# Optimization experiments

Measured on AMD Instinct MI355X. Metric: run time of the kernel, lower is better.

## Reference

```python
import jax, jax.numpy as jnp
import numpy as np
from jax import lax

# dimension numbers for a true 4D convolution: layout is (N, C, s1, s2, s3, s4)
_DN = lax.ConvDimensionNumbers(lhs_spec=(0, 1, 2, 3, 4, 5),
                               rhs_spec=(0, 1, 2, 3, 4, 5),
                               out_spec=(0, 1, 2, 3, 4, 5))


def _conv4d(x, w, b):
    # x: [B, Cin, H1, W1, H2, W2], w: [Cout, Cin, 3, 3, 3, 3], 'same' padding
    y = lax.conv_general_dilated(x, w, window_strides=(1, 1, 1, 1),
                                 padding='SAME', dimension_numbers=_DN)
    return y + b.reshape(1, -1, 1, 1, 1, 1)


def _ncnet(x, W1, b1, W2, b2, W3, b3):
    h = jax.nn.relu(_conv4d(x, W1, b1))
    h = jax.nn.relu(_conv4d(h, W2, b2))
    h = jax.nn.relu(_conv4d(h, W3, b3))
    return h


def setup_inputs() -> dict:
    key = jax.random.key(0)
    ks = jax.random.split(key, 7)
    B, G = 4, 32  # batch, grid size (H1=W1=H2=W2=G)
    x = jax.random.normal(ks[0], (B, 1, G, G, G, G), dtype=jnp.float32)
    s1 = 1.0 / np.sqrt(1 * 3 ** 4)
    s2 = 1.0 / np.sqrt(10 * 3 ** 4)
    W1 = jax.random.normal(ks[1], (10, 1, 3, 3, 3, 3), dtype=jnp.float32) * s1
    b1 = jax.random.normal(ks[2], (10,), dtype=jnp.float32) * s1
    W2 = jax.random.normal(ks[3], (10, 10, 3, 3, 3, 3), dtype=jnp.float32) * s2
    b2 = jax.random.normal(ks[4], (10,), dtype=jnp.float32) * s2
    W3 = jax.random.normal(ks[5], (1, 10, 3, 3, 3, 3), dtype=jnp.float32) * s2
    b3 = jax.random.normal(ks[6], (1,), dtype=jnp.float32) * s2
    return {"x": x, "W1": W1, "b1": b1, "W2": W2, "b2": b2,
            "W3": W3, "b3": b3}


def reference(x, W1, b1, W2, b2, W3, b3):
    # symmetric mode: f(x) + swap(f(swap(x))) where swap exchanges (H1,W1)<->(H2,W2)
    out_a = _ncnet(x, W1, b1, W2, b2, W3, b3)
    xt = jnp.transpose(x, (0, 1, 4, 5, 2, 3))
    out_b = jnp.transpose(_ncnet(xt, W1, b1, W2, b2, W3, b3),
                          (0, 1, 4, 5, 2, 3))
    return out_a + out_b
```

## Files before the change

### kernel.cpp

```cpp
#include <hip/hip_runtime.h>

#define GSZ 32
#define NPTS (1<<20)

#define XB_FLOATS ((size_t)34*34*34*16)
#define XTP ((size_t)34*34*34*160)

#define OFF_XB  ((size_t)0)
#define OFF_X2  (XB_FLOATS)
#define BSLOT   (XB_FLOATS + 4*XTP + 16)

#define WSB_FLOATS 20480
#define NHALO 6536

typedef __attribute__((ext_vector_type(8)))  short bf16x8;
typedef __attribute__((ext_vector_type(16))) float f32x16;
typedef __attribute__((ext_vector_type(4)))  unsigned uintx4;

__device__ __forceinline__ unsigned short f2bf(float f) {
    union { float f; unsigned u; } v; v.f = f;
    unsigned r = v.u + 0x7FFFu + ((v.u >> 16) & 1u);
    return (unsigned short)(r >> 16);
}

__global__ void k_bpack_all(const float* __restrict__ W1, const float* __restrict__ W2,
                            const float* __restrict__ W3,
                            unsigned* __restrict__ wsB2, unsigned* __restrict__ wsB3,
                            unsigned* __restrict__ wsB1) {
    int t = threadIdx.x;
    int lane = t & 63, j = t >> 6;
    int n = lane & 31, kh = lane >> 5;
    for (int br = 0; br < 2; ++br)
        for (int g = 0; g < 27; ++g) {
            int d1 = g / 9, d2 = (g / 3) % 3, d3 = g % 3;
            unsigned v = 0;
            for (int e = 0; e < 2; ++e) {
                int k = kh * 8 + 2 * j + e;
                unsigned short h = 0;
                if (k < 10 && n < 30) {
                    int co = n % 10, d4 = n / 10;
                    int tap = br == 0 ? ((d1 * 3 + d2) * 3 + d3) * 3 + d4
                                      : ((d3 * 3 + d4) * 3 + d1) * 3 + d2;
                    h = f2bf(W2[(co * 10 + k) * 81 + tap]);
                }
                v |= (unsigned)h << (16 * e);
            }
            wsB2[((br * 27 + g) * 64 + lane) * 4 + j] = v;
        }
    for (int br = 0; br < 2; ++br)
        for (int g = 0; g < 9; ++g) {
            int d1 = g / 3, d2 = g % 3;
            unsigned v = 0;
            for (int e = 0; e < 2; ++e) {
                int k = kh * 8 + 2 * j + e;
                unsigned short h = 0;
                if (k < 10 && n < 9) {
                    int d3 = n / 3, d4 = n % 3;
                    int tap = br == 0 ? ((d1 * 3 + d2) * 3 + d3) * 3 + d4
                                      : ((d3 * 3 + d4) * 3 + d1) * 3 + d2;
                    h = f2bf(W3[k * 81 + tap]);
                }
                v |= (unsigned)h << (16 * e);
            }
            wsB3[((br * 9 + g) * 64 + lane) * 4 + j] = v;
        }
    for (int br = 0; br < 2; ++br)
        for (int g = 0; g < 3; ++g) {
            unsigned v = 0;
            for (int e = 0; e < 2; ++e) {
                int kap = kh * 8 + 2 * j + e;
                unsigned short h = 0;
                if (kap < 9 && n < 30) {
                    int co = n % 10, d4 = n / 10;
                    int d1 = kap / 3, d2 = kap % 3;
                    int tap = br == 0 ? ((d1 * 3 + d2) * 3 + g) * 3 + d4
                                      : ((g * 3 + d4) * 3 + d1) * 3 + d2;
                    h = f2bf(W1[co * 81 + tap]);
                }
                v |= (unsigned)h << (16 * e);
            }
            wsB1[((br * 3 + g) * 64 + lane) * 4 + j] = v;
        }
}

__global__ __launch_bounds__(256) void k_zero_halo(float* __restrict__ ws) {
    int wid = blockIdx.x * 4 + (threadIdx.x >> 6);
    if (wid >= NHALO) return;
    int lane = threadIdx.x & 63;
    int i, j, k;
    if (wid < 2312) {
        i = (wid < 1156) ? 0 : 33;
        int r = wid % 1156; j = r / 34; k = r % 34;
    } else if (wid < 4488) {
        int r = wid - 2312;
        i = 1 + r / 68;
        int r2 = r % 68;
        j = (r2 < 34) ? 0 : 33;
        k = r2 % 34;
    } else {
        int r = wid - 4488;
        i = 1 + r / 64;
        int r2 = r % 64;
        j = 1 + (r2 >> 1);
        k = (r2 & 1) ? 33 : 0;
    }
    size_t line = (size_t)(i * 34 + j) * 34 + k;
    float* slot = ws + (size_t)blockIdx.y * BSLOT;
    uintx4 z4 = {0u, 0u, 0u, 0u};
    if (lane < 40) {
        char* base = (char*)(slot + OFF_X2) + line * 640 + lane * 16;
#pragma unroll
        for (int tns = 0; tns < 4; ++tns)
            *(uintx4*)(base + (size_t)tns * (XTP * 4)) = z4;
    }
    if (lane < 4) ((uintx4*)((char*)(slot + OFF_XB) + line * 64))[lane] = z4;
}

__global__ __launch_bounds__(256) void k_copy_in(const float* __restrict__ x,
                                                 float* __restrict__ ws, int b0) {
    int b = b0 + blockIdx.z;
    int gid = blockIdx.x * 256 + threadIdx.x;
    int l0 = (gid & 7) * 4;
    int k = (gid >> 3) & 31, j = (gid >> 8) & 31, i = gid >> 13;
    float4 v = *(const float4*)(x + (size_t)b * NPTS + (size_t)gid * 4);
    ushort4 h;
    h.x = f2bf(v.x); h.y = f2bf(v.y); h.z = f2bf(v.z); h.w = f2bf(v.w);
    unsigned short* XB = (unsigned short*)(ws + (size_t)blockIdx.z * BSLOT + OFF_XB);
    *(ushort4*)(XB + ((size_t)(((i + 1) * 34 + (j + 1)) * 34 + (k + 1))) * 32 + l0) = h;
}

__global__ __launch_bounds__(256) void k_conv1m(const unsigned* __restrict__ wsB1,
                                                const float* __restrict__ B1,
                                                float* ws) {
    __shared__ float epi[4][34 * 33];
    int t = threadIdx.x, lane = t & 63, wv = t >> 6;
    int zb = blockIdx.z >> 2, br = (blockIdx.z >> 1) & 1, w = blockIdx.z & 1;
    int bid = blockIdx.x;
    int s = ((bid & 7) << 7) | (bid >> 3);
    int i = s >> 5, j = s & 31;
    int k0g = w * 16 + wv * 4;
    int q = lane & 31, half = lane >> 5;

    float bias[8];
#pragma unroll
    for (int e = 0; e < 8; ++e) {
        int co = half * 8 + e;
        bias[e] = (co < 10) ? B1[co] : 0.f;
    }
    if (lane < 33) { epi[wv][lane] = 0.f; epi[wv][33 * 33 + lane] = 0.f; }

    float* slot = ws + (size_t)zb * BSLOT;
    const unsigned short* XB = (const unsigned short*)(slot + OFF_XB);
    const unsigned short* xb = XB + ((size_t)((i * 34 + j) * 34 + k0g)) * 32 + q;
    const bf16x8* Bg = (const bf16x8*)(wsB1 + br * 3 * 64 * 4);

    bf16x8 A[6];
    if (half == 0) {
#pragma unroll
        for (int kk = 0; kk < 6; ++kk) {
            bf16x8 a;
#pragma unroll
            for (int e = 0; e < 8; ++e) {
                const int d1 = e / 3, d2 = e % 3;
                a[e] = (short)xb[(size_t)(d1 * 34 + d2) * 1088 + kk * 32];
            }
            A[kk] = a;
        }
    } else {
#pragma unroll
        for (int kk = 0; kk < 6; ++kk) {
            bf16x8 a = {};
            a[0] = (short)xb[(size_t)(2 * 34 + 2) * 1088 + kk * 32];
            A[kk] = a;
        }
    }
    bf16x8 Bf[3];
#pragma unroll
    for (int d3 = 0; d3 < 3; ++d3) Bf[d3] = Bg[d3 * 64 + lane];

    f32x16 D[4] = {};
#pragma unroll
    for (int kk = 0; kk < 6; ++kk)
#pragma unroll
        for (int m = 0; m < 4; ++m) {
            int d3 = kk - m;
            if (d3 >= 0 && d3 < 3)
                D[m] = __builtin_amdgcn_mfma_f32_32x32x16_bf16(A[kk], Bf[d3], D[m], 0, 0, 0);
        }

    float* epw = epi[wv];
    char* X2b = (char*)(slot + OFF_X2 + (size_t)br * XTP);
#pragma unroll
    for (int m = 0; m < 4; ++m) {
#pragma unroll
        for (int r = 0; r < 16; ++r) {
            int row = (r & 3) + 8 * (r >> 2) + 4 * half;
            epw[(row + 1) * 33 + q] = D[m][r];
        }
        size_t lb = ((size_t)(((i + 1) * 34 + (j + 1)) * 34 + (k0g + m + 1))) * 640 + q * 20;
        if (half == 0) {
            unsigned u[4];
#pragma unroll
            for (int e = 0; e < 4; ++e) {
                unsigned short h2[2];
#pragma unroll
                for (int xx = 0; xx < 2; ++xx) {
                    int co = 2 * e + xx;
                    float v = bias[2 * e + xx];
#pragma unroll
                    for (int ss = 0; ss < 3; ++ss)
                        v += epw[(q + ss) * 33 + ss * 10 + co];
                    h2[xx] = f2bf(fmaxf(v, 0.f));
                }
                u[e] = (unsigned)h2[0] | ((unsigned)h2[1] << 16);
            }
            uintx4 u4 = {u[0], u[1], u[2], u[3]};
            *(uintx4*)(X2b + lb) = u4;
        } else {
            unsigned short h2[2];
#pragma unroll
            for (int xx = 0; xx < 2; ++xx) {
                int co = 8 + xx;
                float v = bias[xx];
#pragma unroll
                for (int ss = 0; ss < 3; ++ss)
                    v += epw[(q + ss) * 33 + ss * 10 + co];
                h2[xx] = f2bf(fmaxf(v, 0.f));
            }
            *(unsigned*)(X2b + lb + 16) = (unsigned)h2[0] | ((unsigned)h2[1] << 16);
        }
    }
}

__global__ __launch_bounds__(256) void k_conv2m(const unsigned* __restrict__ wsB,
                                                const float* __restrict__ B2,
                                                float* ws) {
    __shared__ float epi[4][34 * 33];

    int t = threadIdx.x;
    int lane = t & 63, wv = t >> 6;
    int zb = blockIdx.z >> 2, br = (blockIdx.z >> 1) & 1, w = blockIdx.z & 1;
    int bid = blockIdx.x;
    int s = ((bid & 7) << 7) | (bid >> 3);
    int i = s >> 5, j = s & 31;
    int k0 = (w * 4 + wv) * 4;
    int q = lane & 31, half = lane >> 5;

    if (lane < 33) { epi[wv][lane] = 0.f; epi[wv][33 * 33 + lane] = 0.f; }

    float bias[8];
#pragma unroll
    for (int e = 0; e < 8; ++e) {
        int co = half * 8 + e;
        bias[e] = (co < 10) ? B2[co] : 0.f;
    }

    float* slot = ws + (size_t)zb * BSLOT;
    const char* X2b = (const char*)(slot + OFF_X2 + (size_t)br * XTP)
                      + q * 20 + half * 16 + (size_t)k0 * 640;
    const bf16x8* Bg = (const bf16x8*)(wsB + br * 27 * 64 * 4);

    bf16x8 A[2][6];
#pragma unroll
    for (int kk = 0; kk < 6; ++kk)
        A[0][kk] = *(const bf16x8*)(X2b + ((size_t)(i * 34 + j) * 34) * 640 + kk * 640);

    f32x16 D[4] = {};

#pragma unroll
    for (int g = 0; g < 9; ++g) {
        if (g < 8) {
            const int gn = g + 1, d1n = gn / 3, d2n = gn % 3;
            const char* pn = X2b + ((size_t)((i + d1n) * 34 + (j + d2n)) * 34) * 640;
#pragma unroll
            for (int kk = 0; kk < 6; ++kk)
                A[gn & 1][kk] = *(const bf16x8*)(pn + kk * 640);
        }
        bf16x8 Bf[3];
#pragma unroll
        for (int d3 = 0; d3 < 3; ++d3)
            Bf[d3] = Bg[(g * 3 + d3) * 64 + lane];
#pragma unroll
        for (int kk = 0; kk < 6; ++kk)
#pragma unroll
            for (int m = 0; m < 4; ++m) {
                int d3 = kk - m;
                if (d3 >= 0 && d3 < 3)
                    D[m] = __builtin_amdgcn_mfma_f32_32x32x16_bf16(A[g & 1][kk], Bf[d3], D[m], 0, 0, 0);
            }
    }

    float* epw = epi[wv];
    char* X3b = (char*)(slot + OFF_X2 + (size_t)(2 + br) * XTP);
#pragma unroll
    for (int m = 0; m < 4; ++m) {
#pragma unroll
        for (int r = 0; r < 16; ++r) {
            int row = (r & 3) + 8 * (r >> 2) + 4 * half;
            epw[(row + 1) * 33 + q] = D[m][r];
        }
        size_t lb = ((size_t)(((i + 1) * 34 + (j + 1)) * 34 + (k0 + m + 1))) * 640 + q * 20;
        if (half == 0) {
            unsigned u[4];
#pragma unroll
            for (int e = 0; e < 4; ++e) {
                unsigned short h2[2];
#pragma unroll
                for (int xx = 0; xx < 2; ++xx) {
                    int co = 2 * e + xx;
                    float v = bias[2 * e + xx];
#pragma unroll
                    for (int ss = 0; ss < 3; ++ss)
                        v += epw[(q + ss) * 33 + ss * 10 + co];
                    h2[xx] = f2bf(fmaxf(v, 0.f));
                }
                u[e] = (unsigned)h2[0] | ((unsigned)h2[1] << 16);
            }
            uintx4 u4 = {u[0], u[1], u[2], u[3]};
            *(uintx4*)(X3b + lb) = u4;
        } else {
            unsigned short h2[2];
#pragma unroll
            for (int xx = 0; xx < 2; ++xx) {
                int co = 8 + xx;
                float v = bias[xx];
#pragma unroll
                for (int ss = 0; ss < 3; ++ss)
                    v += epw[(q + ss) * 33 + ss * 10 + co];
                h2[xx] = f2bf(fmaxf(v, 0.f));
            }
            *(unsigned*)(X3b + lb + 16) = (unsigned)h2[0] | ((unsigned)h2[1] << 16);
        }
    }
}

__global__ __launch_bounds__(256) void k_conv3m(const unsigned* __restrict__ wsB3,
                                                const float* __restrict__ B3,
                                                float* ws, float* __restrict__ out,
                                                int b0) {
    __shared__ float epi[4][6 * 34 * 9];

    int t = threadIdx.x;
    int lane = t & 63, wv = t >> 6;
    int zb = blockIdx.z >> 1, w = blockIdx.z & 1;
    int b = b0 + zb;
    int bid = blockIdx.x;
    int s = ((bid & 7) << 7) | (bid >> 3);
    int i = s >> 5, j = s & 31;
    int k0 = (w * 4 + wv) * 4;
    int q = lane & 31, half = lane >> 5;

    for (int idx = lane; idx < 6 * 9; idx += 64) {
        int rel = idx / 9, c = idx % 9;
        epi[wv][(rel * 34 + 0) * 9 + c] = 0.f;
        epi[wv][(rel * 34 + 33) * 9 + c] = 0.f;
    }

    float* slot = ws + (size_t)zb * BSLOT;
    float* epw = epi[wv];
    float bb = B3[0];
    float vsum[4];

#pragma unroll 1
    for (int br = 0; br < 2; ++br) {
        const char* X3b = (const char*)(slot + OFF_X2 + (size_t)(2 + br) * XTP)
                          + q * 20 + half * 16 + (size_t)k0 * 640;
        const bf16x8* Bg = (const bf16x8*)(wsB3 + br * 9 * 64 * 4);

        f32x16 D[6] = {};

#pragma unroll 1
        for (int g = 0; g < 9; ++g) {
            const char* pg = X3b + ((size_t)((i + g / 3) * 34 + (j + g % 3)) * 34) * 640;
            bf16x8 Bf = Bg[g * 64 + lane];
#pragma unroll
            for (int rel = 0; rel < 6; ++rel) {
                bf16x8 A = *(const bf16x8*)(pg + rel * 640);
                D[rel] = __builtin_amdgcn_mfma_f32_32x32x16_bf16(A, Bf, D[rel], 0, 0, 0);
            }
        }

        if (q < 9) {
#pragma unroll
            for (int rel = 0; rel < 6; ++rel)
#pragma unroll
                for (int r = 0; r < 16; ++r) {
                    int row = (r & 3) + 8 * (r >> 2) + 4 * half;
                    epw[(rel * 34 + row + 1) * 9 + q] = D[rel][r];
                }
        }
#pragma unroll
        for (int m = 0; m < 4; ++m) {
            float v = bb;
#pragma unroll
            for (int d3 = 0; d3 < 3; ++d3)
#pragma unroll
                for (int d4 = 0; d4 < 3; ++d4)
                    v += epw[((m + d3) * 34 + (q + d4)) * 9 + d3 * 3 + d4];
            v = fmaxf(v, 0.f);
            if (br == 0) vsum[m] = v; else vsum[m] += v;
        }
    }

    float* dst = out + (size_t)b * NPTS;
    if (half == 0)
#pragma unroll
        for (int m = 0; m < 4; ++m)
            dst[(size_t)i * 32768 + j * 1024 + (k0 + m) * 32 + q] = vsum[m];
}

extern "C" void kernel_launch(void* const* d_in, const int* in_sizes, int n_in,
                              void* d_out, int out_size, void* d_ws, size_t ws_size,
                              hipStream_t stream) {
    const float* x  = (const float*)d_in[0];
    const float* W1 = (const float*)d_in[1];
    const float* b1 = (const float*)d_in[2];
    const float* W2 = (const float*)d_in[3];
    const float* b2 = (const float*)d_in[4];
    const float* W3 = (const float*)d_in[5];
    const float* b3 = (const float*)d_in[6];
    float* out = (float*)d_out;
    float* ws  = (float*)d_ws;
    float* slots = ws + WSB_FLOATS;
    unsigned* wsB2 = (unsigned*)ws;
    unsigned* wsB3 = (unsigned*)ws + 13824;
    unsigned* wsB1 = (unsigned*)ws + 18432;

    size_t slot_bytes = BSLOT * sizeof(float);
    int GB = (int)((ws_size - WSB_FLOATS * 4) / slot_bytes);
    if (GB > 4) GB = 4;
    if (GB < 1) GB = 1;

    k_zero_halo<<<dim3((NHALO + 3) / 4, GB), 256, 0, stream>>>(slots);
    k_bpack_all<<<1, 256, 0, stream>>>(W1, W2, W3, wsB2, wsB3, wsB1);

    for (int b0 = 0; b0 < 4; b0 += GB) {
        int gb = 4 - b0 < GB ? 4 - b0 : GB;
        k_copy_in<<<dim3(1024, 1, gb), 256, 0, stream>>>(x, slots, b0);
        k_conv1m<<<dim3(1024, 1, 4 * gb), 256, 0, stream>>>(wsB1, b1, slots);
        k_conv2m<<<dim3(1024, 1, 4 * gb), 256, 0, stream>>>(wsB2, b2, slots);
        k_conv3m<<<dim3(1024, 1, 2 * gb), 256, 0, stream>>>(wsB3, b3, slots, out, b0);
    }
}
```

Baseline: 543.2 us.

## Stage conv1 input through shared memory and split conv2 into more blocks

```diff
diff --git a/kernel.cpp b/kernel.cpp
--- a/kernel.cpp
+++ b/kernel.cpp
@@ -132,14 +132,31 @@
 __global__ __launch_bounds__(256) void k_conv1m(const unsigned* __restrict__ wsB1,
                                                 const float* __restrict__ B1,
                                                 float* ws) {
+    __shared__ __align__(16) unsigned char stg[18 * 640 + 16];
     __shared__ float epi[4][34 * 33];
     int t = threadIdx.x, lane = t & 63, wv = t >> 6;
     int zb = blockIdx.z >> 2, br = (blockIdx.z >> 1) & 1, w = blockIdx.z & 1;
     int bid = blockIdx.x;
     int s = ((bid & 7) << 7) | (bid >> 3);
     int i = s >> 5, j = s & 31;
-    int k0g = w * 16 + wv * 4;
     int q = lane & 31, half = lane >> 5;
+
+    float* slot = ws + (size_t)zb * BSLOT;
+    const unsigned short* XB = (const unsigned short*)(slot + OFF_XB);
+
+    for (int c = t; c < 648; c += 256) {
+        int d = c / 72, rem = c % 72;
+        int kl = rem >> 2, l0 = (rem & 3) * 8;
+        const unsigned short* src = XB
+            + ((size_t)((i + d / 3) * 34 + (j + d % 3)) * 34 + (w * 16 + kl)) * 32 + l0;
+        bf16x8 v = *(const bf16x8*)src;
+#pragma unroll
+        for (int x8 = 0; x8 < 8; ++x8)
+            *(unsigned short*)(stg + kl * 640 + (l0 + x8) * 20 + d * 2) = (unsigned short)v[x8];
+    }
+    for (int idx = t; idx < 576; idx += 256)
+        *(unsigned short*)(stg + (idx >> 5) * 640 + (idx & 31) * 20 + 18) = 0;
+    if (t < 8) *(unsigned short*)(stg + 11520 + t * 2) = 0;
 
     float bias[8];
 #pragma unroll
@@ -148,32 +165,15 @@
         bias[e] = (co < 10) ? B1[co] : 0.f;
     }
     if (lane < 33) { epi[wv][lane] = 0.f; epi[wv][33 * 33 + lane] = 0.f; }
-
-    float* slot = ws + (size_t)zb * BSLOT;
-    const unsigned short* XB = (const unsigned short*)(slot + OFF_XB);
-    const unsigned short* xb = XB + ((size_t)((i * 34 + j) * 34 + k0g)) * 32 + q;
+    __syncthreads();
+
+    int k0g = w * 16 + wv * 4;
     const bf16x8* Bg = (const bf16x8*)(wsB1 + br * 3 * 64 * 4);
 
     bf16x8 A[6];
-    if (half == 0) {
-#pragma unroll
-        for (int kk = 0; kk < 6; ++kk) {
-            bf16x8 a;
-#pragma unroll
-            for (int e = 0; e < 8; ++e) {
-                const int d1 = e / 3, d2 = e % 3;
-                a[e] = (short)xb[(size_t)(d1 * 34 + d2) * 1088 + kk * 32];
-            }
-            A[kk] = a;
-        }
-    } else {
-#pragma unroll
-        for (int kk = 0; kk < 6; ++kk) {
-            bf16x8 a = {};
-            a[0] = (short)xb[(size_t)(2 * 34 + 2) * 1088 + kk * 32];
-            A[kk] = a;
-        }
-    }
+#pragma unroll
+    for (int kk = 0; kk < 6; ++kk)
+        A[kk] = *(const bf16x8*)(stg + (wv * 4 + kk) * 640 + q * 20 + half * 16);
     bf16x8 Bf[3];
 #pragma unroll
     for (int d3 = 0; d3 < 3; ++d3) Bf[d3] = Bg[d3 * 64 + lane];
@@ -239,11 +239,11 @@
 
     int t = threadIdx.x;
     int lane = t & 63, wv = t >> 6;
-    int zb = blockIdx.z >> 2, br = (blockIdx.z >> 1) & 1, w = blockIdx.z & 1;
+    int zb = blockIdx.z >> 3, br = (blockIdx.z >> 2) & 1, qz = blockIdx.z & 3;
     int bid = blockIdx.x;
     int s = ((bid & 7) << 7) | (bid >> 3);
     int i = s >> 5, j = s & 31;
-    int k0 = (w * 4 + wv) * 4;
+    int k0 = qz * 8 + wv * 2;
     int q = lane & 31, half = lane >> 5;
 
     if (lane < 33) { epi[wv][lane] = 0.f; epi[wv][33 * 33 + lane] = 0.f; }
@@ -260,12 +260,12 @@
                       + q * 20 + half * 16 + (size_t)k0 * 640;
     const bf16x8* Bg = (const bf16x8*)(wsB + br * 27 * 64 * 4);
 
-    bf16x8 A[2][6];
-#pragma unroll
-    for (int kk = 0; kk < 6; ++kk)
+    bf16x8 A[2][4];
+#pragma unroll
+    for (int kk = 0; kk < 4; ++kk)
         A[0][kk] = *(const bf16x8*)(X2b + ((size_t)(i * 34 + j) * 34) * 640 + kk * 640);
 
-    f32x16 D[4] = {};
+    f32x16 D[2] = {};
 
 #pragma unroll
     for (int g = 0; g < 9; ++g) {
@@ -273,7 +273,7 @@
             const int gn = g + 1, d1n = gn / 3, d2n = gn % 3;
             const char* pn = X2b + ((size_t)((i + d1n) * 34 + (j + d2n)) * 34) * 640;
 #pragma unroll
-            for (int kk = 0; kk < 6; ++kk)
+            for (int kk = 0; kk < 4; ++kk)
                 A[gn & 1][kk] = *(const bf16x8*)(pn + kk * 640);
         }
         bf16x8 Bf[3];
@@ -281,9 +281,9 @@
         for (int d3 = 0; d3 < 3; ++d3)
             Bf[d3] = Bg[(g * 3 + d3) * 64 + lane];
 #pragma unroll
-        for (int kk = 0; kk < 6; ++kk)
-#pragma unroll
-            for (int m = 0; m < 4; ++m) {
+        for (int kk = 0; kk < 4; ++kk)
+#pragma unroll
+            for (int m = 0; m < 2; ++m) {
                 int d3 = kk - m;
                 if (d3 >= 0 && d3 < 3)
                     D[m] = __builtin_amdgcn_mfma_f32_32x32x16_bf16(A[g & 1][kk], Bf[d3], D[m], 0, 0, 0);
@@ -293,7 +293,7 @@
     float* epw = epi[wv];
     char* X3b = (char*)(slot + OFF_X2 + (size_t)(2 + br) * XTP);
 #pragma unroll
-    for (int m = 0; m < 4; ++m) {
+    for (int m = 0; m < 2; ++m) {
 #pragma unroll
         for (int r = 0; r < 16; ++r) {
             int row = (r & 3) + 8 * (r >> 2) + 4 * half;
@@ -438,7 +438,7 @@
         int gb = 4 - b0 < GB ? 4 - b0 : GB;
         k_copy_in<<<dim3(1024, 1, gb), 256, 0, stream>>>(x, slots, b0);
         k_conv1m<<<dim3(1024, 1, 4 * gb), 256, 0, stream>>>(wsB1, b1, slots);
-        k_conv2m<<<dim3(1024, 1, 4 * gb), 256, 0, stream>>>(wsB2, b2, slots);
+        k_conv2m<<<dim3(1024, 1, 8 * gb), 256, 0, stream>>>(wsB2, b2, slots);
         k_conv3m<<<dim3(1024, 1, 2 * gb), 256, 0, stream>>>(wsB3, b3, slots, out, b0);
     }
 }
```

Result: slower. 587.8 us (+8.2%).
